# Kernel tuning notes

Hardware: AMD Instinct MI355X
Metric: run time of the kernel (lower is better)

Reference implementation:

```python
import jax, jax.numpy as jnp
import numpy as np

N, B, E, D, DQ, H = 20000, 32, 320000, 128, 1024, 2
L = N // B  # 625 nodes per graph (equal-size graphs -> static max_node_num)
NUM_GNN_LAYERS = 3


def setup_inputs() -> dict:
    key = jax.random.key(0)
    ks = jax.random.split(key, 32)
    rn = lambda k, s, scale=1.0: jax.random.normal(k, s, jnp.float32) * scale
    w = lambda k, fi, fo: rn(k, (fi, fo), 1.0 / np.sqrt(fi))
    inp = {
        'x': rn(ks[0], (N, D)),
        'edge_attr': rn(ks[1], (E, D)),
        'u': rn(ks[2], (B, D)),
        'qa_attr': rn(ks[3], (B, DQ)),
        # edge MLP: cat(src,dest,edge_attr,u[eb]) = 4D -> hidden D -> D
        'W_e1': w(ks[4], 4 * D, D), 'b_e1': jnp.zeros((D,)),
        'W_e2': w(ks[5], D, D), 'b_e2': jnp.zeros((D,)),
        # weight mlp: cat(edge_attr, u[eb]) = 2D -> 1 (num_layers=1)
        'W_w': w(ks[6], 2 * D, 1), 'b_w': jnp.zeros((1,)),
        # message mlp: cat(x[row], edge_attr) = 2D -> D -> D
        'W_m1': w(ks[7], 2 * D, D), 'b_m1': jnp.zeros((D,)),
        'W_m2': w(ks[8], D, D), 'b_m2': jnp.zeros((D,)),
        # update mlp: cat(x, received, u[nb]) = 3D -> D -> D
        'W_u1': w(ks[9], 3 * D, D), 'b_u1': jnp.zeros((D,)),
        'W_u2': w(ks[10], D, D), 'b_u2': jnp.zeros((D,)),
        # multihead att-pool: q from qa_attr (DQ) -> H*dk; k,v from evidence (D) -> H*dk
        'W_q': w(ks[11], DQ, D), 'b_q': jnp.zeros((D,)),
        'W_k': w(ks[12], D, D), 'b_k': jnp.zeros((D,)),
        'W_v': w(ks[13], D, D), 'b_v': jnp.zeros((D,)),
        'edge_index': jax.random.randint(ks[14], (2, E), 0, N, dtype=jnp.int32),
        'node_batch': (jnp.arange(N, dtype=jnp.int32) // L).astype(jnp.int32),
        'num_of_nodes': jnp.full((B,), L, dtype=jnp.int32),
    }
    return inp


def _mlp2(h, W1, b1, W2, b2):
    return jax.nn.relu(h @ W1 + b1) @ W2 + b2


def _seg_softmax(logits, seg, num):
    m = jax.ops.segment_max(logits, seg, num_segments=num)
    e = jnp.exp(logits - m[seg])
    s = jax.ops.segment_sum(e, seg, num_segments=num)
    return e / s[seg]


def reference(x, edge_attr, u, qa_attr,
              W_e1, b_e1, W_e2, b_e2, W_w, b_w,
              W_m1, b_m1, W_m2, b_m2, W_u1, b_u1, W_u2, b_u2,
              W_q, b_q, W_k, b_k, W_v, b_v,
              edge_index, node_batch, num_of_nodes):
    row, col = edge_index[0], edge_index[1]
    edge_batch = node_batch[row]
    Bsz, Nn = u.shape[0], x.shape[0]
    Lm = Nn // Bsz  # static max_node_num (equal-size graphs)

    norm_w = None
    for _ in range(NUM_GNN_LAYERS):
        ue = u[edge_batch]  # [E, D]
        # EdgeModel: cat(src, dest, edge_attr, u[eb]) -> MLP -> new edge_attr
        new_edge = _mlp2(jnp.concatenate([x[row], x[col], edge_attr, ue], 1),
                         W_e1, b_e1, W_e2, b_e2)
        # edge weights from OLD edge_attr (per EdgeV1Model.forward)
        wts = jnp.concatenate([edge_attr, ue], 1) @ W_w + b_w  # [E,1]
        norm_w = _seg_softmax(wts[:, 0], edge_batch, Bsz)[:, None]  # [E,1]
        edge_attr = new_edge
        # NodeModel: message MLP, weighted scatter_mean over col, update MLP
        msg = _mlp2(jnp.concatenate([x[row], edge_attr], 1), W_m1, b_m1, W_m2, b_m2)
        summed = jax.ops.segment_sum(msg * norm_w, col, num_segments=Nn)
        cnt = jax.ops.segment_sum(jnp.ones((msg.shape[0],), msg.dtype), col, num_segments=Nn)
        received = summed / jnp.maximum(cnt, 1.0)[:, None]
        x = _mlp2(jnp.concatenate([x, received, u[node_batch]], 1),
                  W_u1, b_u1, W_u2, b_u2)

    pooled_edge = jax.ops.segment_sum(edge_attr * norm_w, edge_batch, num_segments=Bsz)  # [B,D]
    # evidence packing: equal graphs -> simple reshape, then exact GELU
    evidence = jax.nn.gelu(x.reshape(Bsz, Lm, -1), approximate=False)  # [B,L,D]
    mask = jnp.arange(Lm)[None, :] >= num_of_nodes[:, None]  # [B,L] True = masked

    # MultiheadAttPoolLayer
    dk = W_k.shape[1] // H
    q = (qa_attr @ W_q + b_q).reshape(Bsz, H, dk)
    k = (evidence @ W_k + b_k).reshape(Bsz, Lm, H, dk)
    v = (evidence @ W_v + b_v).reshape(Bsz, Lm, H, dk)
    scores = jnp.einsum('bhd,blhd->bhl', q, k) / jnp.sqrt(jnp.float32(dk))
    scores = jnp.where(mask[:, None, :], -1e30, scores)
    attn = jax.nn.softmax(scores, axis=-1)
    pooled_node = jnp.einsum('bhl,blhd->bhd', attn, v).reshape(Bsz, H * dk)  # [B,D]

    return jnp.concatenate([pooled_edge, pooled_node], 1)  # [B, 2D]
```

## Files before the change

### kernel.cpp

```cpp
#include <hip/hip_runtime.h>
#include <math.h>

typedef __bf16 bf16_t;
typedef bf16_t bf16x8 __attribute__((ext_vector_type(8)));
typedef bf16_t bf16x4 __attribute__((ext_vector_type(4)));
typedef bf16_t bf16x2 __attribute__((ext_vector_type(2)));
typedef float  f32x4  __attribute__((ext_vector_type(4)));

#define N_NODES 20000
#define NEDGE   320000
#define DIM     128
#define TP      136
#define EBLK    2500
#define FBLK    10000
#define NBLK    625
#define GPRE    157

#define FE1  0
#define FE2  49152
#define FM1  65536
#define FM2  98304
#define FU1  114688
#define FU2  163840
#define FK   180224
#define FV   196608
#define WF_ELEMS 212992

__device__ __forceinline__ void acc_zero32(f32x4 acc[2][8]) {
  f32x4 z = {0.f, 0.f, 0.f, 0.f};
#pragma unroll
  for (int i = 0; i < 2; ++i)
#pragma unroll
    for (int j = 0; j < 8; ++j) acc[i][j] = z;
}

__device__ __forceinline__ void wstage_rows_bf(bf16_t* sA, const bf16_t* src, int rowreg, int lane) {
  int r = lane >> 1, h = lane & 1;
  int row = __shfl(rowreg, r);
  const bf16_t* sp = src + (size_t)row * DIM + h * 64;
  bf16_t* dp = sA + r * TP + h * 64;
#pragma unroll
  for (int i = 0; i < 8; ++i)
    *(uint4*)(dp + i * 8) = *(const uint4*)(sp + i * 8);
}

__device__ __forceinline__ void wstage_rows_f32(bf16_t* sA, const float* src, int rowreg, int lane) {
  int r = lane >> 1, h = lane & 1;
  int row = __shfl(rowreg, r);
  const float* sp = src + (size_t)row * DIM + h * 64;
  bf16_t* dp = sA + r * TP + h * 64;
#pragma unroll
  for (int i = 0; i < 8; ++i) {
    float4 f0 = *(const float4*)(sp + i * 8);
    float4 f1 = *(const float4*)(sp + i * 8 + 4);
    bf16x8 tv;
    tv[0]=(bf16_t)f0.x; tv[1]=(bf16_t)f0.y; tv[2]=(bf16_t)f0.z; tv[3]=(bf16_t)f0.w;
    tv[4]=(bf16_t)f1.x; tv[5]=(bf16_t)f1.y; tv[6]=(bf16_t)f1.z; tv[7]=(bf16_t)f1.w;
    *(bf16x8*)(dp + i * 8) = tv;
  }
}

__device__ __forceinline__ void wstage_seq_bf(bf16_t* sA, const bf16_t* src, int base, int lane) {
  int r = lane >> 1, h = lane & 1;
  const bf16_t* sp = src + (size_t)(base + r) * DIM + h * 64;
  bf16_t* dp = sA + r * TP + h * 64;
#pragma unroll
  for (int i = 0; i < 8; ++i)
    *(uint4*)(dp + i * 8) = *(const uint4*)(sp + i * 8);
}

__device__ __forceinline__ void wstage_seq_f32(bf16_t* sA, const float* src, int base, int lane) {
  int r = lane >> 1, h = lane & 1;
  const float* sp = src + (size_t)(base + r) * DIM + h * 64;
  bf16_t* dp = sA + r * TP + h * 64;
#pragma unroll
  for (int i = 0; i < 8; ++i) {
    float4 f0 = *(const float4*)(sp + i * 8);
    float4 f1 = *(const float4*)(sp + i * 8 + 4);
    bf16x8 tv;
    tv[0]=(bf16_t)f0.x; tv[1]=(bf16_t)f0.y; tv[2]=(bf16_t)f0.z; tv[3]=(bf16_t)f0.w;
    tv[4]=(bf16_t)f1.x; tv[5]=(bf16_t)f1.y; tv[6]=(bf16_t)f1.z; tv[7]=(bf16_t)f1.w;
    *(bf16x8*)(dp + i * 8) = tv;
  }
}

__device__ __forceinline__ void chunk_stage(bf16_t* ch, const bf16_t* __restrict__ src, int t) {
#pragma unroll
  for (int i = 0; i < 8; ++i) {
    int idx = (i * 256 + t) * 8;
    *(uint4*)(ch + idx) = *(const uint4*)(src + idx);
  }
}

__device__ __forceinline__ void wmfma_lds(const bf16_t* sA, const bf16_t* ch,
                                          int lane, int lm, int lq, f32x4 acc[2][8]) {
#pragma unroll
  for (int kk = 0; kk < 4; ++kk) {
    int ko = kk * 32 + lq * 8;
    bf16x8 a0 = *(const bf16x8*)(sA + lm * TP + ko);
    bf16x8 a1 = *(const bf16x8*)(sA + (16 + lm) * TP + ko);
    const bf16_t* wp = ch + (kk << 12) + (lane << 3);
#pragma unroll
    for (int ct = 0; ct < 8; ++ct) {
      bf16x8 bfr = *(const bf16x8*)(wp + (ct << 9));
      acc[0][ct] = __builtin_amdgcn_mfma_f32_16x16x32_bf16(a0, bfr, acc[0][ct], 0, 0, 0);
      acc[1][ct] = __builtin_amdgcn_mfma_f32_16x16x32_bf16(a1, bfr, acc[1][ct], 0, 0, 0);
    }
  }
}

__device__ __forceinline__ void wmfma_gk128(const bf16_t* sA, const bf16_t* __restrict__ Wf,
                                            int lane, int lm, int lq, f32x4 acc[2][8]) {
#pragma unroll
  for (int kk = 0; kk < 4; ++kk) {
    int ko = kk * 32 + lq * 8;
    bf16x8 a0 = *(const bf16x8*)(sA + lm * TP + ko);
    bf16x8 a1 = *(const bf16x8*)(sA + (16 + lm) * TP + ko);
    const bf16_t* wp = Wf + ((kk * 8) << 9) + (lane << 3);
#pragma unroll
    for (int ct = 0; ct < 8; ++ct) {
      bf16x8 bfr = *(const bf16x8*)(wp + (ct << 9));
      acc[0][ct] = __builtin_amdgcn_mfma_f32_16x16x32_bf16(a0, bfr, acc[0][ct], 0, 0, 0);
      acc[1][ct] = __builtin_amdgcn_mfma_f32_16x16x32_bf16(a1, bfr, acc[1][ct], 0, 0, 0);
    }
  }
}

__device__ __forceinline__ void merge_shfl(float& m, float& s, int width) {
  for (int k = 1; k < width; k <<= 1) {
    float m2 = __shfl_xor(m, k), s2 = __shfl_xor(s, k);
    float M = fmaxf(m, m2), ns = 0.f;
    if (m  > -1e29f) ns += s  * expf(m  - M);
    if (m2 > -1e29f) ns += s2 * expf(m2 - M);
    m = M; s = ns;
  }
}

__global__ void gn_xcvt(const float* x, bf16_t* xb) {
  int i = blockIdx.x * 256 + threadIdx.x;
  if (i < N_NODES * DIM / 4) {
    float4 f = ((const float4*)x)[i];
    bf16x4 o; o[0]=(bf16_t)f.x; o[1]=(bf16_t)f.y; o[2]=(bf16_t)f.z; o[3]=(bf16_t)f.w;
    *(bf16x4*)(xb + (size_t)i * 4) = o;
  }
}

__global__ void gn_fragw(const float* We1, const float* We2, const float* Wm1, const float* Wm2,
                         const float* Wu1, const float* Wu2, const float* Wk, const float* Wv,
                         bf16_t* WF) {
  int idx = blockIdx.x * 256 + threadIdx.x;
  if (idx >= WF_ELEMS) return;
  int seg = idx >> 14;
  const float* W; int kc;
  switch (seg) {
    case 0:  W = We1; kc = 0; break;
    case 1:  W = We1; kc = 1; break;
    case 2:  W = We1; kc = 2; break;
    case 3:  W = We2; kc = 0; break;
    case 4:  W = Wm1; kc = 0; break;
    case 5:  W = Wm1; kc = 1; break;
    case 6:  W = Wm2; kc = 0; break;
    case 7:  W = Wu1; kc = 0; break;
    case 8:  W = Wu1; kc = 1; break;
    case 9:  W = Wu1; kc = 2; break;
    case 10: W = Wu2; kc = 0; break;
    case 11: W = Wk;  kc = 0; break;
    default: W = Wv;  kc = 0; break;
  }
  int r = idx & 16383;
  int j = r & 7, lane = (r >> 3) & 63, ct = (r >> 9) & 7, kk = (r >> 12) & 3;
  int k = kc * 128 + kk * 32 + (lane >> 4) * 8 + j;
  int n = ct * 16 + (lane & 15);
  WF[idx] = (bf16_t)W[k * 128 + n];
}

__global__ void gn_uprep(const float* u, const float* We1, const float* be1,
                         const float* Ww, const float* bw, float* R, float* uw) {
  int t = threadIdx.x;
  for (int idx = blockIdx.x * 256 + t; idx < 32 * 128; idx += gridDim.x * 256) {
    int g = idx >> 7, c = idx & 127;
    float acc = be1[c];
    for (int k = 0; k < 128; ++k) acc += u[g * 128 + k] * We1[(384 + k) * 128 + c];
    R[idx] = acc;
  }
  if (blockIdx.x == 0 && t < 32) {
    float acc = bw[0];
    for (int k = 0; k < 128; ++k) acc += u[t * 128 + k] * Ww[128 + k];
    uw[t] = acc;
  }
}

__global__ void gn_counti(const int* ei, int* cnti) {
  int e = blockIdx.x * 256 + threadIdx.x;
  if (e < NEDGE) atomicAdd(&cnti[ei[NEDGE + e]], 1);
}

__global__ void gn_scan(const int* cnti, int* off, int* curs) {
  __shared__ int part[256];
  int t = threadIdx.x;
  int base = t * 80;
  int lim = base + 80; if (lim > N_NODES) lim = N_NODES;
  int s = 0;
  for (int i = base; i < lim; ++i) s += cnti[i];
  part[t] = s;
  __syncthreads();
  for (int d = 1; d < 256; d <<= 1) {
    int add = (t >= d) ? part[t - d] : 0;
    __syncthreads();
    part[t] += add;
    __syncthreads();
  }
  int pfx = (t == 0) ? 0 : part[t - 1];
  for (int i = base; i < lim; ++i) {
    off[i] = pfx; curs[i] = pfx; pfx += cnti[i];
  }
  if (t == 0) off[N_NODES] = NEDGE;
}

__global__ void gn_eidx(const int* ei, int* curs, int* eidx) {
  int e = blockIdx.x * 256 + threadIdx.x;
  if (e < NEDGE) {
    int c = ei[NEDGE + e];
    int pos = atomicAdd(&curs[c], 1);
    eidx[pos] = e;
  }
}

__global__ void gn_q(const float* qa, const float* Wq, const float* bq, float* qb) {
  int b = blockIdx.x, t = threadIdx.x;
  int c = t & 127, half = t >> 7;
  const float* qrow = qa + b * 1024 + half * 512;
  float acc = 0.f;
  for (int k = 0; k < 512; ++k) acc += qrow[k] * Wq[(half * 512 + k) * 128 + c];
  __shared__ float red[256];
  red[t] = acc;
  __syncthreads();
  if (half == 0) qb[b * 128 + c] = red[c] + red[128 + c] + bq[c];
}

__global__ void gn_wl0(const float* ea, const float* Ww, const float* uw,
                       const int* ei, const int* nbat, float* wl, int* gb) {
  int t = threadIdx.x;
  int sub = t & 15, grp = t >> 4;
  for (int e = blockIdx.x * 16 + grp; e < NEDGE; e += gridDim.x * 16) {
    const float* er = ea + (size_t)e * DIM + sub * 8;
    float s = 0.f;
#pragma unroll
    for (int j = 0; j < 8; ++j) s += er[j] * Ww[sub * 8 + j];
#pragma unroll
    for (int m = 1; m < 16; m <<= 1) s += __shfl_xor(s, m);
    if (sub == 0) {
      int g = nbat[ei[e]];
      wl[e] = s + uw[g];
      gb[e] = g;
    }
  }
}

__global__ void gn_part0(const float* wl, const int* gb, float* pm, float* ps) {
  __shared__ float lv[128];
  __shared__ int   lgg[128];
  int t = threadIdx.x, blk = blockIdx.x, e0 = blk * 128;
  if (t < 128) { lv[t] = wl[e0 + t]; lgg[t] = gb[e0 + t]; }
  __syncthreads();
  int g = t >> 3, seg = t & 7;
  float m = -1e30f, s = 0.f;
  for (int i = seg * 16; i < seg * 16 + 16; ++i)
    if (lgg[i] == g) {
      float v = lv[i];
      if (v > m) { s = s * expf(m - v) + 1.f; m = v; }
      else s += expf(v - m);
    }
  merge_shfl(m, s, 8);
  if (seg == 0) { pm[blk * 32 + g] = m; ps[blk * 32 + g] = s; }
}

__global__ void gn_reduce_ms(const float* pm, const float* ps, float* mg, float* sg, int nb) {
  int g = blockIdx.x, t = threadIdx.x;
  __shared__ float red[256];
  float m = -1e30f;
  for (int i = t; i < nb; i += 256) m = fmaxf(m, pm[i * 32 + g]);
  red[t] = m; __syncthreads();
  for (int s2 = 128; s2 > 0; s2 >>= 1) { if (t < s2) red[t] = fmaxf(red[t], red[t + s2]); __syncthreads(); }
  m = red[0]; __syncthreads();
  float s = 0.f;
  for (int i = t; i < nb; i += 256) {
    float sb = ps[i * 32 + g];
    if (sb > 0.f) s += sb * expf(pm[i * 32 + g] - m);
  }
  red[t] = s; __syncthreads();
  for (int s2 = 128; s2 > 0; s2 >>= 1) { if (t < s2) red[t] += red[t + s2]; __syncthreads(); }
  if (t == 0) { mg[g] = m; sg[g] = red[0]; }
}

__global__ __launch_bounds__(256, 2) void gn_fused(
    const bf16_t* __restrict__ xb,
    const void* esrcv, int efirst,
    bf16_t* edst,
    const bf16_t* __restrict__ WF,
    const float* R, const float* UW, const float* Wwv,
    const float* be2, const float* bm1, const float* bm2,
    const float* wl_cur, const float* mg, const float* sg,
    float* wl_next, float* pm, float* ps, int last,
    const int* ei, const int* gb, bf16_t* msg,
    const float* uu, const float* bu1, const int* nbat, float* pre) {
  __shared__ bf16_t chunk[16384];
  __shared__ bf16_t band[4][32 * TP];
  __shared__ float slwt[128];

  int t = threadIdx.x;
  int w = t >> 6, lane = t & 63;
  int lm = lane & 15, lq = lane >> 4;
  int blk = blockIdx.x;
  bf16_t* myband = band[w];

  if (blk >= EBLK) {
    int nb128 = blk - EBLK;
    int gb32 = nb128 * 4 + w;
    int lrow = 0, lgr = 0;
    if (lane < 32) {
      int node = gb32 * 32 + lane;
      if (node > N_NODES - 1) node = N_NODES - 1;
      lrow = node;
      lgr = nbat[node];
    }
    f32x4 acc[2][8];
    acc_zero32(acc);
    wstage_rows_bf(myband, xb, lrow, lane);
    chunk_stage(chunk, WF + FU1, t);
    __syncthreads();
    wmfma_lds(myband, chunk, lane, lm, lq, acc);
    __syncthreads();
    wstage_rows_f32(myband, uu, lgr, lane);
    chunk_stage(chunk, WF + FU1 + 32768, t);
    __syncthreads();
    wmfma_lds(myband, chunk, lane, lm, lq, acc);
    if (gb32 < NBLK) {
      float* pp = pre + (size_t)gb32 * 4096 + lane * 64;
#pragma unroll
      for (int rt = 0; rt < 2; ++rt)
#pragma unroll
        for (int reg = 0; reg < 4; ++reg)
#pragma unroll
          for (int ct = 0; ct < 8; ++ct)
            pp[rt * 32 + reg * 8 + ct] = acc[rt][ct][reg] + bu1[ct * 16 + lm];
    }
    return;
  }

  int e0 = blk * 128;
  int ew0 = e0 + w * 32;
  int lrowr = 0, lcolr = 0, lgr = 0;
  float lnwr = 0.f;
  if (lane < 32) {
    int e = ew0 + lane;
    lrowr = ei[e];
    lcolr = ei[NEDGE + e];
    lgr = gb[e];
    lnwr = expf(wl_cur[e] - mg[lgr]) / sg[lgr];
  }

  f32x4 accE[2][8], accM[2][8];
  acc_zero32(accE);
  acc_zero32(accM);

  wstage_rows_bf(myband, xb, lrowr, lane);
  chunk_stage(chunk, WF + FE1, t);
  __syncthreads();
  wmfma_lds(myband, chunk, lane, lm, lq, accE);
  __syncthreads();
  chunk_stage(chunk, WF + FM1, t);
  __syncthreads();
  wmfma_lds(myband, chunk, lane, lm, lq, accM);
  __syncthreads();
  wstage_rows_bf(myband, xb, lcolr, lane);
  chunk_stage(chunk, WF + FE1 + 16384, t);
  __syncthreads();
  wmfma_lds(myband, chunk, lane, lm, lq, accE);
  __syncthreads();
  if (efirst) wstage_seq_f32(myband, (const float*)esrcv, ew0, lane);
  else        wstage_seq_bf (myband, (const bf16_t*)esrcv, ew0, lane);
  chunk_stage(chunk, WF + FE1 + 32768, t);
  __syncthreads();
  wmfma_lds(myband, chunk, lane, lm, lq, accE);
  __syncthreads();

  {
#pragma unroll
    for (int rt = 0; rt < 2; ++rt)
#pragma unroll
      for (int reg = 0; reg < 4; ++reg) {
        int row = rt * 16 + lq * 4 + reg;
        const float* Rr = R + (size_t)__shfl(lgr, row) * DIM;
#pragma unroll
        for (int ct = 0; ct < 8; ++ct) {
          int col = ct * 16 + lm;
          myband[row * TP + col] = (bf16_t)fmaxf(accE[rt][ct][reg] + Rr[col], 0.f);
        }
      }
  }
  acc_zero32(accE);
  chunk_stage(chunk, WF + FE2, t);
  __syncthreads();
  wmfma_lds(myband, chunk, lane, lm, lq, accE);
  __syncthreads();

  {
    float ww8[8], be8[8];
#pragma unroll
    for (int ct = 0; ct < 8; ++ct) { ww8[ct] = Wwv[ct * 16 + lm]; be8[ct] = be2[ct * 16 + lm]; }
#pragma unroll
    for (int rt = 0; rt < 2; ++rt)
#pragma unroll
      for (int reg = 0; reg < 4; ++reg) {
        int row = rt * 16 + lq * 4 + reg;
        int g = __shfl(lgr, row);
        bf16_t* drow = edst + (size_t)(ew0 + row) * DIM;
        float lsum = 0.f;
#pragma unroll
        for (int ct = 0; ct < 8; ++ct) {
          int col = ct * 16 + lm;
          float v = accE[rt][ct][reg] + be8[ct];
          drow[col] = (bf16_t)v;
          myband[row * TP + col] = (bf16_t)v;
          lsum += v * ww8[ct];
        }
        if (!last) {
          lsum += __shfl_xor(lsum, 1);
          lsum += __shfl_xor(lsum, 2);
          lsum += __shfl_xor(lsum, 4);
          lsum += __shfl_xor(lsum, 8);
          if (lm == 0) {
            float v2 = lsum + UW[g];
            wl_next[ew0 + row] = v2;
            slwt[w * 32 + row] = v2;
          }
        }
      }
  }
  chunk_stage(chunk, WF + FM1 + 16384, t);
  __syncthreads();
  wmfma_lds(myband, chunk, lane, lm, lq, accM);
  __syncthreads();

  {
    float bm18[8];
#pragma unroll
    for (int ct = 0; ct < 8; ++ct) bm18[ct] = bm1[ct * 16 + lm];
#pragma unroll
    for (int rt = 0; rt < 2; ++rt)
#pragma unroll
      for (int reg = 0; reg < 4; ++reg) {
        int row = rt * 16 + lq * 4 + reg;
#pragma unroll
        for (int ct = 0; ct < 8; ++ct) {
          int col = ct * 16 + lm;
          myband[row * TP + col] = (bf16_t)fmaxf(accM[rt][ct][reg] + bm18[ct], 0.f);
        }
      }
  }
  acc_zero32(accM);
  chunk_stage(chunk, WF + FM2, t);
  __syncthreads();
  wmfma_lds(myband, chunk, lane, lm, lq, accM);

  {
    float bm28[8];
#pragma unroll
    for (int ct = 0; ct < 8; ++ct) bm28[ct] = bm2[ct * 16 + lm];
#pragma unroll
    for (int rt = 0; rt < 2; ++rt)
#pragma unroll
      for (int reg = 0; reg < 4; ++reg) {
        int row = rt * 16 + lq * 4 + reg;
        float nwv = __shfl(lnwr, row);
#pragma unroll
        for (int ct = 0; ct < 8; ++ct) {
          int col = ct * 16 + lm;
          myband[row * TP + col] = (bf16_t)((accM[rt][ct][reg] + bm28[ct]) * nwv);
        }
      }
    int r = lane >> 1, h = lane & 1;
    bf16_t* dp = msg + (size_t)(ew0 + r) * DIM + h * 64;
    const bf16_t* sp = myband + r * TP + h * 64;
#pragma unroll
    for (int i = 0; i < 8; ++i)
      *(uint4*)(dp + i * 8) = *(const uint4*)(sp + i * 8);
  }

  if (!last) {
    int g = lane >> 1, seg = lane & 1;
    float m = -1e30f, s = 0.f;
    for (int i = seg * 16; i < seg * 16 + 16; ++i) {
      int gi = __shfl(lgr, i);
      if (gi == g) {
        float v = slwt[w * 32 + i];
        if (v > m) { s = s * expf(m - v) + 1.f; m = v; }
        else s += expf(v - m);
      }
    }
    merge_shfl(m, s, 2);
    if (seg == 0) { pm[(blk * 4 + w) * 32 + g] = m; ps[(blk * 4 + w) * 32 + g] = s; }
  }
}

__global__ __launch_bounds__(256) void gn_gather(
    const bf16_t* __restrict__ msg, const int* __restrict__ off,
    const int* __restrict__ eidx, bf16_t* recvb) {
  int w = threadIdx.x >> 6, lane = threadIdx.x & 63;
  int n = blockIdx.x * 4 + w;
  int o0 = off[n], o1 = off[n + 1];
  float a0 = 0.f, a1 = 0.f;
  int i = o0;
  int e = (i < o1) ? eidx[i] : 0;
  for (; i < o1; ++i) {
    int en = (i + 1 < o1) ? eidx[i + 1] : 0;
    bf16x2 v = *(const bf16x2*)(msg + (size_t)e * DIM + lane * 2);
    a0 += (float)v[0];
    a1 += (float)v[1];
    e = en;
  }
  float ic = 1.f / fmaxf((float)(o1 - o0), 1.f);
  bf16x2 o; o[0] = (bf16_t)(a0 * ic); o[1] = (bf16_t)(a1 * ic);
  *(bf16x2*)(recvb + (size_t)n * DIM + lane * 2) = o;
}

__global__ __launch_bounds__(64, 3) void gn_node(
    bf16_t* xdst, const bf16_t* recvb, const float* pre,
    const bf16_t* __restrict__ WF, const float* bu2) {
  __shared__ bf16_t sA[32 * TP];

  int lane = threadIdx.x;
  int nb = blockIdx.x;
  int n0 = nb * 32;
  int lm = lane & 15, lq = lane >> 4;

  wstage_seq_bf(sA, recvb, n0, lane);

  f32x4 acc[2][8];
  acc_zero32(acc);
  wmfma_gk128(sA, WF + FU1 + 16384, lane, lm, lq, acc);

  const float* pp = pre + (size_t)nb * 4096 + lane * 64;
#pragma unroll
  for (int rt = 0; rt < 2; ++rt)
#pragma unroll
    for (int reg = 0; reg < 4; ++reg) {
      int row = rt * 16 + lq * 4 + reg;
#pragma unroll
      for (int ct = 0; ct < 8; ++ct) {
        int col = ct * 16 + lm;
        sA[row * TP + col] = (bf16_t)fmaxf(acc[rt][ct][reg] + pp[rt * 32 + reg * 8 + ct], 0.f);
      }
    }
  acc_zero32(acc);
  wmfma_gk128(sA, WF + FU2, lane, lm, lq, acc);

  {
    float bu28[8];
#pragma unroll
    for (int ct = 0; ct < 8; ++ct) bu28[ct] = bu2[ct * 16 + lm];
#pragma unroll
    for (int rt = 0; rt < 2; ++rt)
#pragma unroll
      for (int reg = 0; reg < 4; ++reg) {
        int row = rt * 16 + lq * 4 + reg;
        bf16_t* dr = xdst + (size_t)(n0 + row) * DIM;
#pragma unroll
        for (int ct = 0; ct < 8; ++ct) {
          int col = ct * 16 + lm;
          dr[col] = (bf16_t)(acc[rt][ct][reg] + bu28[ct]);
        }
      }
  }
}

__global__ __launch_bounds__(64, 3) void gn_ev(
    const bf16_t* xsrc, const bf16_t* __restrict__ WF,
    const float* bk, const float* bv, float* kb, float* vb) {
  __shared__ bf16_t sA[32 * TP];

  int lane = threadIdx.x;
  int n0 = blockIdx.x * 32;
  int sel = blockIdx.y;
  const bf16_t* Wf = WF + (sel ? FV : FK);
  const float* bias = sel ? bv : bk;
  float* dst = sel ? vb : kb;
  int lm = lane & 15, lq = lane >> 4;

  {
    int r = lane >> 1, h = lane & 1;
    const bf16_t* sp = xsrc + (size_t)(n0 + r) * DIM + h * 64;
    bf16_t* dp = sA + r * TP + h * 64;
#pragma unroll
    for (int i = 0; i < 8; ++i) {
      uint4 v = *(const uint4*)(sp + i * 8);
      bf16_t tmp[8];
      *(uint4*)tmp = v;
      bf16x8 tv;
#pragma unroll
      for (int j = 0; j < 8; ++j) {
        float f = (float)tmp[j];
        tv[j] = (bf16_t)(0.5f * f * (1.f + erff(f * 0.70710678118654752f)));
      }
      *(bf16x8*)(dp + i * 8) = tv;
    }
  }

  f32x4 acc[2][8];
  acc_zero32(acc);
  wmfma_gk128(sA, Wf, lane, lm, lq, acc);

  {
    float b8[8];
#pragma unroll
    for (int ct = 0; ct < 8; ++ct) b8[ct] = bias[ct * 16 + lm];
#pragma unroll
    for (int rt = 0; rt < 2; ++rt)
#pragma unroll
      for (int reg = 0; reg < 4; ++reg) {
        int row = rt * 16 + lq * 4 + reg;
        float* dr = dst + (size_t)(n0 + row) * DIM;
#pragma unroll
        for (int ct = 0; ct < 8; ++ct) {
          int col = ct * 16 + lm;
          dr[col] = acc[rt][ct][reg] + b8[ct];
        }
      }
  }
}

__global__ void gn_pooled_edge(const bf16_t* eb, const float* wl, const float* mg, const float* sg,
                               const int* gb, float* pe) {
  __shared__ float loc[4096];
  int t = threadIdx.x;
  for (int i = t; i < 4096; i += 256) loc[i] = 0.f;
  __syncthreads();
  int lane = t & 63, w = t >> 6;
  int wid = blockIdx.x * 4 + w, nw = gridDim.x * 4;
  for (int e = wid; e < NEDGE; e += nw) {
    int g = gb[e];
    float nwt = expf(wl[e] - mg[g]) / sg[g];
    const bf16_t* er = eb + (size_t)e * DIM + lane * 2;
    atomicAdd(&loc[g * 128 + lane * 2],     (float)er[0] * nwt);
    atomicAdd(&loc[g * 128 + lane * 2 + 1], (float)er[1] * nwt);
  }
  __syncthreads();
  for (int i = t; i < 4096; i += 256) atomicAdd(&pe[i], loc[i]);
}

__global__ void gn_att(const float* qb, const float* kb, const float* vb, const int* non, float* out) {
  int b = blockIdx.x >> 1, h = blockIdx.x & 1, t = threadIdx.x;
  __shared__ float qv[64];
  __shared__ float sc[625];
  __shared__ float red[256];
  if (t < 64) qv[t] = qb[b * 128 + h * 64 + t];
  __syncthreads();
  int nn = non[b];
  for (int l = t; l < 625; l += 256) {
    float acc = 0.f;
    const float* kr = kb + ((size_t)(b * 625 + l)) * DIM + h * 64;
    for (int d2 = 0; d2 < 64; ++d2) acc += qv[d2] * kr[d2];
    sc[l] = (l < nn) ? acc * 0.125f : -1e30f;
  }
  __syncthreads();
  float m = -1e30f;
  for (int l = t; l < 625; l += 256) m = fmaxf(m, sc[l]);
  red[t] = m; __syncthreads();
  for (int s2 = 128; s2 > 0; s2 >>= 1) { if (t < s2) red[t] = fmaxf(red[t], red[t + s2]); __syncthreads(); }
  m = red[0]; __syncthreads();
  float ssum = 0.f;
  for (int l = t; l < 625; l += 256) { float e = expf(sc[l] - m); sc[l] = e; ssum += e; }
  red[t] = ssum; __syncthreads();
  for (int s2 = 128; s2 > 0; s2 >>= 1) { if (t < s2) red[t] += red[t + s2]; __syncthreads(); }
  float inv = 1.f / red[0];
  __syncthreads();
  int d = t & 63, seg = t >> 6;
  float acc = 0.f;
  for (int l = seg; l < 625; l += 4) acc += sc[l] * vb[((size_t)(b * 625 + l)) * DIM + h * 64 + d];
  red[t] = acc; __syncthreads();
  if (t < 64) {
    float v = red[t] + red[64 + t] + red[128 + t] + red[192 + t];
    out[b * 256 + 128 + h * 64 + d] = v * inv;
  }
}

__global__ void gn_fin(const float* pe, float* out) {
  int t = threadIdx.x;
  for (int i = t; i < 4096; i += 256) {
    int b = i >> 7, c = i & 127;
    out[b * 256 + c] = pe[i];
  }
}

extern "C" void kernel_launch(void* const* d_in, const int* in_sizes, int n_in,
                              void* d_out, int out_size, void* d_ws, size_t ws_size,
                              hipStream_t stream) {
  const float* x   = (const float*)d_in[0];
  const float* ea  = (const float*)d_in[1];
  const float* u   = (const float*)d_in[2];
  const float* qa  = (const float*)d_in[3];
  const float* We1 = (const float*)d_in[4];
  const float* be1 = (const float*)d_in[5];
  const float* We2 = (const float*)d_in[6];
  const float* be2 = (const float*)d_in[7];
  const float* Ww  = (const float*)d_in[8];
  const float* bw  = (const float*)d_in[9];
  const float* Wm1 = (const float*)d_in[10];
  const float* bm1 = (const float*)d_in[11];
  const float* Wm2 = (const float*)d_in[12];
  const float* bm2 = (const float*)d_in[13];
  const float* Wu1 = (const float*)d_in[14];
  const float* bu1 = (const float*)d_in[15];
  const float* Wu2 = (const float*)d_in[16];
  const float* bu2 = (const float*)d_in[17];
  const float* Wq  = (const float*)d_in[18];
  const float* bq  = (const float*)d_in[19];
  const float* Wk  = (const float*)d_in[20];
  const float* bk  = (const float*)d_in[21];
  const float* Wv  = (const float*)d_in[22];
  const float* bv  = (const float*)d_in[23];
  const int* ei   = (const int*)d_in[24];
  const int* nbat = (const int*)d_in[25];
  const int* non  = (const int*)d_in[26];
  float* out = (float*)d_out;

  char* p = (char*)d_ws;
  auto alloc = [&](size_t bytes) { char* r = p; p += (bytes + 255) & ~(size_t)255; return r; };
  bf16_t* EB    = (bf16_t*)alloc((size_t)NEDGE * DIM * 2);
  bf16_t* XB    = (bf16_t*)alloc((size_t)N_NODES * DIM * 2);
  bf16_t* XB0   = (bf16_t*)alloc((size_t)N_NODES * DIM * 2);
  bf16_t* MSG   = (bf16_t*)alloc((size_t)NEDGE * DIM * 2);
  bf16_t* RECVB = (bf16_t*)alloc((size_t)N_NODES * DIM * 2);
  int*   CNTI = (int*)alloc((size_t)N_NODES * 4);
  int*   OFF  = (int*)alloc((size_t)(N_NODES + 1) * 4);
  int*   CURS = (int*)alloc((size_t)N_NODES * 4);
  int*   EIDX = (int*)alloc((size_t)NEDGE * 4);
  float* WL   = (float*)alloc((size_t)NEDGE * 4);
  float* WLn  = (float*)alloc((size_t)NEDGE * 4);
  int*   GB   = (int*)alloc((size_t)NEDGE * 4);
  float* PM   = (float*)alloc((size_t)FBLK * 32 * 4);
  float* PS   = (float*)alloc((size_t)FBLK * 32 * 4);
  float* MG   = (float*)alloc(32 * 4);
  float* SG   = (float*)alloc(32 * 4);
  float* R    = (float*)alloc(32 * 128 * 4);
  float* UW   = (float*)alloc(32 * 4);
  bf16_t* WF  = (bf16_t*)alloc((size_t)WF_ELEMS * 2);
  float* QB   = (float*)alloc(32 * 128 * 4);
  float* KB   = (float*)alloc((size_t)N_NODES * DIM * 4);
  float* VB   = (float*)alloc((size_t)N_NODES * DIM * 4);
  float* PE   = (float*)alloc(32 * 128 * 4);
  float* PRE  = (float*)alloc((size_t)N_NODES * DIM * 4);

  hipMemsetAsync(CNTI, 0, (size_t)N_NODES * 4, stream);
  hipMemsetAsync(PE, 0, 32 * 128 * 4, stream);

  gn_xcvt<<<(N_NODES * DIM / 4 + 255) / 256, 256, 0, stream>>>(x, XB0);
  gn_fragw<<<(WF_ELEMS + 255) / 256, 256, 0, stream>>>(We1, We2, Wm1, Wm2, Wu1, Wu2, Wk, Wv, WF);
  gn_uprep<<<16, 256, 0, stream>>>(u, We1, be1, Ww, bw, R, UW);
  gn_counti<<<1250, 256, 0, stream>>>(ei, CNTI);
  gn_scan<<<1, 256, 0, stream>>>(CNTI, OFF, CURS);
  gn_eidx<<<1250, 256, 0, stream>>>(ei, CURS, EIDX);
  gn_q<<<32, 256, 0, stream>>>(qa, Wq, bq, QB);
  gn_wl0<<<2500, 256, 0, stream>>>(ea, Ww, UW, ei, nbat, WL, GB);
  gn_part0<<<EBLK, 256, 0, stream>>>(WL, GB, PM, PS);

  for (int layer = 0; layer < 3; ++layer) {
    int first = (layer == 0) ? 1 : 0;
    int last = (layer == 2) ? 1 : 0;
    const bf16_t* xs = first ? XB0 : XB;
    const void* es = first ? (const void*)ea : (const void*)EB;
    float* cur = (layer == 1) ? WLn : WL;
    float* nxt = (layer == 1) ? WL : WLn;
    gn_reduce_ms<<<32, 256, 0, stream>>>(PM, PS, MG, SG, first ? EBLK : FBLK);
    gn_fused<<<EBLK + GPRE, 256, 0, stream>>>(xs, es, first, EB, WF, R, UW, Ww,
                                              be2, bm1, bm2, cur, MG, SG,
                                              nxt, PM, PS, last, ei, GB, MSG,
                                              u, bu1, nbat, PRE);
    gn_gather<<<5000, 256, 0, stream>>>(MSG, OFF, EIDX, RECVB);
    gn_node<<<NBLK, 64, 0, stream>>>(XB, RECVB, PRE, WF, bu2);
  }

  gn_pooled_edge<<<256, 256, 0, stream>>>(EB, WL, MG, SG, GB, PE);
  gn_ev<<<dim3(NBLK, 2), 64, 0, stream>>>(XB, WF, bk, bv, KB, VB);
  gn_att<<<64, 256, 0, stream>>>(QB, KB, VB, non, out);
  gn_fin<<<1, 256, 0, stream>>>(PE, out);
}
```

Baseline: 1.573 ms.

## Prefetch weight chunks into registers to overlap with MFMA in fused edge kernel

The fused edge kernel now loads the next weight chunk from global memory into registers before running the current MFMA stage, then writes it to LDS after a barrier, so weight fetch latency overlaps compute. Edge-feature stores are coalesced through the LDS band as 16-byte vector writes, the per-graph bias R is permuted so each lane fetches its eight values with two float4 loads, and the PRE buffer layout is transposed for coalesced access. The attention score loop also uses float4 loads. The register prefetch adds 32 VGPRs per thread, which may lower occupancy under launch bounds of 2 blocks.

```diff
diff --git a/kernel.cpp b/kernel.cpp
--- a/kernel.cpp
+++ b/kernel.cpp
@@ -175,13 +175,13 @@
 }
 
 __global__ void gn_uprep(const float* u, const float* We1, const float* be1,
-                         const float* Ww, const float* bw, float* R, float* uw) {
+                         const float* Ww, const float* bw, float* Rp, float* uw) {
   int t = threadIdx.x;
   for (int idx = blockIdx.x * 256 + t; idx < 32 * 128; idx += gridDim.x * 256) {
     int g = idx >> 7, c = idx & 127;
     float acc = be1[c];
     for (int k = 0; k < 128; ++k) acc += u[g * 128 + k] * We1[(384 + k) * 128 + c];
-    R[idx] = acc;
+    Rp[g * 128 + (c & 15) * 8 + (c >> 4)] = acc;
   }
   if (blockIdx.x == 0 && t < 32) {
     float acc = bw[0];
@@ -298,7 +298,7 @@
     const void* esrcv, int efirst,
     bf16_t* edst,
     const bf16_t* __restrict__ WF,
-    const float* R, const float* UW, const float* Wwv,
+    const float* Rp, const float* UW, const float* Wwv,
     const float* be2, const float* bm1, const float* bm2,
     const float* wl_cur, const float* mg, const float* sg,
     float* wl_next, float* pm, float* ps, int last,
@@ -336,14 +336,14 @@
     __syncthreads();
     wmfma_lds(myband, chunk, lane, lm, lq, acc);
     if (gb32 < NBLK) {
-      float* pp = pre + (size_t)gb32 * 4096 + lane * 64;
+      float* pp = pre + (size_t)gb32 * 4096 + lane;
 #pragma unroll
       for (int rt = 0; rt < 2; ++rt)
 #pragma unroll
         for (int reg = 0; reg < 4; ++reg)
 #pragma unroll
           for (int ct = 0; ct < 8; ++ct)
-            pp[rt * 32 + reg * 8 + ct] = acc[rt][ct][reg] + bu1[ct * 16 + lm];
+            pp[((rt * 32 + reg * 8 + ct) << 6)] = acc[rt][ct][reg] + bu1[ct * 16 + lm];
     }
     return;
   }
@@ -364,47 +364,64 @@
   acc_zero32(accE);
   acc_zero32(accM);
 
+  uint4 c0, c1, c2, c3, c4, c5, c6, c7;
+#define CLOAD(SRC) { const uint4* _s = (const uint4*)(SRC) + t; \
+  c0 = _s[0];    c1 = _s[256];  c2 = _s[512];  c3 = _s[768]; \
+  c4 = _s[1024]; c5 = _s[1280]; c6 = _s[1536]; c7 = _s[1792]; }
+#define CWRITE() { uint4* _d = (uint4*)chunk + t; \
+  _d[0] = c0;    _d[256] = c1;  _d[512] = c2;  _d[768] = c3; \
+  _d[1024] = c4; _d[1280] = c5; _d[1536] = c6; _d[1792] = c7; }
+
+  CLOAD(WF + FE1);
   wstage_rows_bf(myband, xb, lrowr, lane);
-  chunk_stage(chunk, WF + FE1, t);
-  __syncthreads();
+  CWRITE();
+  __syncthreads();
+
+  CLOAD(WF + FM1);
   wmfma_lds(myband, chunk, lane, lm, lq, accE);
   __syncthreads();
-  chunk_stage(chunk, WF + FM1, t);
-  __syncthreads();
+  CWRITE();
+  __syncthreads();
+
+  CLOAD(WF + FE1 + 16384);
   wmfma_lds(myband, chunk, lane, lm, lq, accM);
-  __syncthreads();
   wstage_rows_bf(myband, xb, lcolr, lane);
-  chunk_stage(chunk, WF + FE1 + 16384, t);
-  __syncthreads();
+  __syncthreads();
+  CWRITE();
+  __syncthreads();
+
+  CLOAD(WF + FE1 + 32768);
   wmfma_lds(myband, chunk, lane, lm, lq, accE);
-  __syncthreads();
   if (efirst) wstage_seq_f32(myband, (const float*)esrcv, ew0, lane);
   else        wstage_seq_bf (myband, (const bf16_t*)esrcv, ew0, lane);
-  chunk_stage(chunk, WF + FE1 + 32768, t);
-  __syncthreads();
+  __syncthreads();
+  CWRITE();
+  __syncthreads();
+
+  CLOAD(WF + FE2);
   wmfma_lds(myband, chunk, lane, lm, lq, accE);
-  __syncthreads();
-
-  {
-#pragma unroll
-    for (int rt = 0; rt < 2; ++rt)
-#pragma unroll
-      for (int reg = 0; reg < 4; ++reg) {
-        int row = rt * 16 + lq * 4 + reg;
-        const float* Rr = R + (size_t)__shfl(lgr, row) * DIM;
-#pragma unroll
-        for (int ct = 0; ct < 8; ++ct) {
-          int col = ct * 16 + lm;
-          myband[row * TP + col] = (bf16_t)fmaxf(accE[rt][ct][reg] + Rr[col], 0.f);
-        }
+#pragma unroll
+  for (int rt = 0; rt < 2; ++rt)
+#pragma unroll
+    for (int reg = 0; reg < 4; ++reg) {
+      int row = rt * 16 + lq * 4 + reg;
+      int g = __shfl(lgr, row);
+      const float4* rp = (const float4*)(Rp + (size_t)g * 128 + lm * 8);
+      float4 ra = rp[0], rb = rp[1];
+      float rv[8] = {ra.x, ra.y, ra.z, ra.w, rb.x, rb.y, rb.z, rb.w};
+#pragma unroll
+      for (int ct = 0; ct < 8; ++ct) {
+        int col = ct * 16 + lm;
+        myband[row * TP + col] = (bf16_t)fmaxf(accE[rt][ct][reg] + rv[ct], 0.f);
       }
-  }
+    }
   acc_zero32(accE);
-  chunk_stage(chunk, WF + FE2, t);
-  __syncthreads();
+  __syncthreads();
+  CWRITE();
+  __syncthreads();
+
+  CLOAD(WF + FM1 + 16384);
   wmfma_lds(myband, chunk, lane, lm, lq, accE);
-  __syncthreads();
-
   {
     float ww8[8], be8[8];
 #pragma unroll
@@ -415,13 +432,11 @@
       for (int reg = 0; reg < 4; ++reg) {
         int row = rt * 16 + lq * 4 + reg;
         int g = __shfl(lgr, row);
-        bf16_t* drow = edst + (size_t)(ew0 + row) * DIM;
         float lsum = 0.f;
 #pragma unroll
         for (int ct = 0; ct < 8; ++ct) {
           int col = ct * 16 + lm;
           float v = accE[rt][ct][reg] + be8[ct];
-          drow[col] = (bf16_t)v;
           myband[row * TP + col] = (bf16_t)v;
           lsum += v * ww8[ct];
         }
@@ -437,12 +452,19 @@
           }
         }
       }
-  }
-  chunk_stage(chunk, WF + FM1 + 16384, t);
-  __syncthreads();
+    int r = lane >> 1, h = lane & 1;
+    bf16_t* dp = edst + (size_t)(ew0 + r) * DIM + h * 64;
+    const bf16_t* sp2 = myband + r * TP + h * 64;
+#pragma unroll
+    for (int i = 0; i < 8; ++i)
+      *(uint4*)(dp + i * 8) = *(const uint4*)(sp2 + i * 8);
+  }
+  __syncthreads();
+  CWRITE();
+  __syncthreads();
+
+  CLOAD(WF + FM2);
   wmfma_lds(myband, chunk, lane, lm, lq, accM);
-  __syncthreads();
-
   {
     float bm18[8];
 #pragma unroll
@@ -460,10 +482,11 @@
       }
   }
   acc_zero32(accM);
-  chunk_stage(chunk, WF + FM2, t);
-  __syncthreads();
+  __syncthreads();
+  CWRITE();
+  __syncthreads();
+
   wmfma_lds(myband, chunk, lane, lm, lq, accM);
-
   {
     float bm28[8];
 #pragma unroll
@@ -482,10 +505,10 @@
       }
     int r = lane >> 1, h = lane & 1;
     bf16_t* dp = msg + (size_t)(ew0 + r) * DIM + h * 64;
-    const bf16_t* sp = myband + r * TP + h * 64;
+    const bf16_t* sp2 = myband + r * TP + h * 64;
 #pragma unroll
     for (int i = 0; i < 8; ++i)
-      *(uint4*)(dp + i * 8) = *(const uint4*)(sp + i * 8);
+      *(uint4*)(dp + i * 8) = *(const uint4*)(sp2 + i * 8);
   }
 
   if (!last) {
@@ -502,6 +525,8 @@
     merge_shfl(m, s, 2);
     if (seg == 0) { pm[(blk * 4 + w) * 32 + g] = m; ps[(blk * 4 + w) * 32 + g] = s; }
   }
+#undef CLOAD
+#undef CWRITE
 }
 
 __global__ __launch_bounds__(256) void gn_gather(
@@ -541,7 +566,7 @@
   acc_zero32(acc);
   wmfma_gk128(sA, WF + FU1 + 16384, lane, lm, lq, acc);
 
-  const float* pp = pre + (size_t)nb * 4096 + lane * 64;
+  const float* pp = pre + (size_t)nb * 4096 + lane;
 #pragma unroll
   for (int rt = 0; rt < 2; ++rt)
 #pragma unroll
@@ -550,7 +575,7 @@
 #pragma unroll
       for (int ct = 0; ct < 8; ++ct) {
         int col = ct * 16 + lm;
-        sA[row * TP + col] = (bf16_t)fmaxf(acc[rt][ct][reg] + pp[rt * 32 + reg * 8 + ct], 0.f);
+        sA[row * TP + col] = (bf16_t)fmaxf(acc[rt][ct][reg] + pp[((rt * 32 + reg * 8 + ct) << 6)], 0.f);
       }
     }
   acc_zero32(acc);
@@ -657,10 +682,16 @@
   if (t < 64) qv[t] = qb[b * 128 + h * 64 + t];
   __syncthreads();
   int nn = non[b];
+  const float4* qv4 = (const float4*)qv;
   for (int l = t; l < 625; l += 256) {
     float acc = 0.f;
-    const float* kr = kb + ((size_t)(b * 625 + l)) * DIM + h * 64;
-    for (int d2 = 0; d2 < 64; ++d2) acc += qv[d2] * kr[d2];
+    const float4* kr = (const float4*)(kb + ((size_t)(b * 625 + l)) * DIM + h * 64);
+#pragma unroll
+    for (int d2 = 0; d2 < 16; ++d2) {
+      float4 kv = kr[d2];
+      float4 qq = qv4[d2];
+      acc += qq.x * kv.x + qq.y * kv.y + qq.z * kv.z + qq.w * kv.w;
+    }
     sc[l] = (l < nn) ? acc * 0.125f : -1e30f;
   }
   __syncthreads();
@@ -743,7 +774,7 @@
   float* PS   = (float*)alloc((size_t)FBLK * 32 * 4);
   float* MG   = (float*)alloc(32 * 4);
   float* SG   = (float*)alloc(32 * 4);
-  float* R    = (float*)alloc(32 * 128 * 4);
+  float* RP   = (float*)alloc(32 * 128 * 4);
   float* UW   = (float*)alloc(32 * 4);
   bf16_t* WF  = (bf16_t*)alloc((size_t)WF_ELEMS * 2);
   float* QB   = (float*)alloc(32 * 128 * 4);
@@ -757,7 +788,7 @@
 
   gn_xcvt<<<(N_NODES * DIM / 4 + 255) / 256, 256, 0, stream>>>(x, XB0);
   gn_fragw<<<(WF_ELEMS + 255) / 256, 256, 0, stream>>>(We1, We2, Wm1, Wm2, Wu1, Wu2, Wk, Wv, WF);
-  gn_uprep<<<16, 256, 0, stream>>>(u, We1, be1, Ww, bw, R, UW);
+  gn_uprep<<<16, 256, 0, stream>>>(u, We1, be1, Ww, bw, RP, UW);
   gn_counti<<<1250, 256, 0, stream>>>(ei, CNTI);
   gn_scan<<<1, 256, 0, stream>>>(CNTI, OFF, CURS);
   gn_eidx<<<1250, 256, 0, stream>>>(ei, CURS, EIDX);
@@ -773,7 +804,7 @@
     float* cur = (layer == 1) ? WLn : WL;
     float* nxt = (layer == 1) ? WL : WLn;
     gn_reduce_ms<<<32, 256, 0, stream>>>(PM, PS, MG, SG, first ? EBLK : FBLK);
-    gn_fused<<<EBLK + GPRE, 256, 0, stream>>>(xs, es, first, EB, WF, R, UW, Ww,
+    gn_fused<<<EBLK + GPRE, 256, 0, stream>>>(xs, es, first, EB, WF, RP, UW, Ww,
                                               be2, bm1, bm2, cur, MG, SG,
                                               nxt, PM, PS, last, ei, GB, MSG,
                                               u, bu1, nbat, PRE);
```

Measured after the change: 1.475 ms. -6.2%, faster.
